# Performance work log

Measured on AMD Instinct MI355X. Metric: run time of the kernel, lower is better.

## Reference

```python
import jax, jax.numpy as jnp
import numpy as np

BATCH, SEQ, IN_DIM, UNITS = 64, 2048, 256, 256


def _glorot(key, shape):
    lim = np.sqrt(6.0 / (shape[0] + shape[1]))
    return jax.random.uniform(key, shape, jnp.float32, -lim, lim)


def setup_inputs() -> dict:
    key = jax.random.key(0)
    ks = jax.random.split(key, 5)
    return {
        "inputs": jax.random.normal(ks[0], (BATCH, SEQ, IN_DIM), jnp.float32),
        "W_f": _glorot(ks[1], (IN_DIM, UNITS)),
        "U_f": _glorot(ks[2], (UNITS, UNITS)),
        "b_f": jnp.zeros((UNITS,), jnp.float32),
        "W_s": _glorot(ks[3], (IN_DIM, UNITS)),
        "U_s": _glorot(ks[4], (UNITS, UNITS)),
        "b_s": jnp.zeros((UNITS,), jnp.float32),
    }


def reference(inputs, W_f, U_f, b_f, W_s, U_s, b_s):
    # Precompute input projections for all timesteps (one big GEMM each).
    xf = jnp.einsum('bti,iu->btu', inputs, W_f) + b_f  # (B, T, U)
    xs = jnp.einsum('bti,iu->btu', inputs, W_s) + b_s  # (B, T, U)

    h0 = jnp.zeros((inputs.shape[0], U_f.shape[0]), inputs.dtype)

    def step(h, xt):
        xf_t, xs_t = xt
        f_t = jax.nn.sigmoid(xf_t + h @ U_f)
        s_tilde = jnp.tanh(xs_t + (f_t * h) @ U_s)
        h_new = (1.0 - f_t) * h + f_t * s_tilde
        return h_new, h_new

    # scan over time: move time axis to front
    _, hs = jax.lax.scan(step, h0, (jnp.swapaxes(xf, 0, 1), jnp.swapaxes(xs, 0, 1)))
    return jnp.swapaxes(hs, 0, 1)  # (B, T, U)
```

## Files before the change

### kernel.cpp

```cpp
#include <hip/hip_runtime.h>
#include <hip/hip_bf16.h>

#define BATCH 64
#define SEQ 2048
#define IN_DIM 256
#define UNITS 256

typedef _Float16 half2_t __attribute__((ext_vector_type(2)));

__device__ __forceinline__ float fdot2(half2_t a, half2_t b, float c) {
#if __has_builtin(__builtin_amdgcn_fdot2)
    return __builtin_amdgcn_fdot2(a, b, c, false);
#else
    return c + (float)a[0] * (float)b[0] + (float)a[1] * (float)b[1];
#endif
}

__device__ __forceinline__ void lds_barrier() {
    asm volatile("s_waitcnt lgkmcnt(0)" ::: "memory");
    __builtin_amdgcn_s_barrier();
    asm volatile("" ::: "memory");
}

__global__ void prep_u(const float* __restrict__ Uf, const float* __restrict__ Us,
                       _Float16* __restrict__ Utf, _Float16* __restrict__ Uts) {
    int idx = blockIdx.x * 256 + threadIdx.x;
    int k = idx >> 8;
    int u = idx & 255;
    Utf[u * 256 + k] = (_Float16)Uf[idx];
    Uts[u * 256 + k] = (_Float16)Us[idx];
}

__global__ __launch_bounds__(256) void proj_kernel(
    const float* __restrict__ X,
    const float* __restrict__ Wf, const float* __restrict__ bf,
    const float* __restrict__ Wsm, const float* __restrict__ bs,
    float* __restrict__ xf_out, _Float16* __restrict__ xs_out)
{
    __shared__ float Xs[64][65];
    __shared__ float Wsh[64][68];

    const int tid = threadIdx.x;
    const int rt = blockIdx.x;
    const int ct = blockIdx.y;
    const int r0 = rt * 64;
    const bool is_f = ct < 4;
    const int c0 = (ct & 3) * 64;
    const float* W = is_f ? Wf : Wsm;
    const float* bias = is_f ? bf : bs;
    const int tx = tid & 15;
    const int ty = tid >> 4;

    float acc[4][4];
#pragma unroll
    for (int i = 0; i < 4; ++i)
#pragma unroll
        for (int j = 0; j < 4; ++j) acc[i][j] = 0.f;

    for (int kc = 0; kc < IN_DIM; kc += 64) {
        __syncthreads();
#pragma unroll
        for (int i = 0; i < 4; ++i) {
            int f = tid + i * 256;
            int row = f >> 4;
            int kq = f & 15;
            float4 v = *(const float4*)(X + (size_t)(r0 + row) * IN_DIM + kc + kq * 4);
            Xs[row][kq * 4 + 0] = v.x;
            Xs[row][kq * 4 + 1] = v.y;
            Xs[row][kq * 4 + 2] = v.z;
            Xs[row][kq * 4 + 3] = v.w;
        }
#pragma unroll
        for (int i = 0; i < 4; ++i) {
            int f = tid + i * 256;
            int kk = f >> 4;
            int n4 = f & 15;
            float4 v = *(const float4*)(W + (size_t)(kc + kk) * UNITS + c0 + n4 * 4);
            *(float4*)&Wsh[kk][n4 * 4] = v;
        }
        __syncthreads();
#pragma unroll 8
        for (int kk = 0; kk < 64; ++kk) {
            float a0 = Xs[tx * 4 + 0][kk];
            float a1 = Xs[tx * 4 + 1][kk];
            float a2 = Xs[tx * 4 + 2][kk];
            float a3 = Xs[tx * 4 + 3][kk];
            float4 bv = *(const float4*)&Wsh[kk][ty * 4];
            acc[0][0] += a0 * bv.x; acc[0][1] += a0 * bv.y; acc[0][2] += a0 * bv.z; acc[0][3] += a0 * bv.w;
            acc[1][0] += a1 * bv.x; acc[1][1] += a1 * bv.y; acc[1][2] += a1 * bv.z; acc[1][3] += a1 * bv.w;
            acc[2][0] += a2 * bv.x; acc[2][1] += a2 * bv.y; acc[2][2] += a2 * bv.z; acc[2][3] += a2 * bv.w;
            acc[3][0] += a3 * bv.x; acc[3][1] += a3 * bv.y; acc[3][2] += a3 * bv.z; acc[3][3] += a3 * bv.w;
        }
    }

#pragma unroll
    for (int i = 0; i < 4; ++i) {
        int r = r0 + tx * 4 + i;
        int n0 = c0 + ty * 4;
        if (is_f) {
            float4 v;
            v.x = acc[i][0] + bias[n0 + 0];
            v.y = acc[i][1] + bias[n0 + 1];
            v.z = acc[i][2] + bias[n0 + 2];
            v.w = acc[i][3] + bias[n0 + 3];
            *(float4*)(xf_out + (size_t)r * UNITS + n0) = v;
        } else {
#pragma unroll
            for (int j = 0; j < 4; ++j)
                xs_out[(size_t)r * UNITS + n0 + j] = (_Float16)(acc[i][j] + bias[n0 + j]);
        }
    }
}

__global__ __launch_bounds__(512, 1) void recur_kernel(
    float* xf_out,
    const _Float16* __restrict__ xs16,
    const _Float16* __restrict__ Utf,
    const _Float16* __restrict__ Uts)
{
    __shared__ __align__(16) _Float16 h2[256];
    __shared__ __align__(16) _Float16 g2[256];

    const int tid = threadIdx.x;
    const int u = tid >> 1;
    const int q = tid & 1;
    const int b = blockIdx.x;

    union F4H { float4 f4; half2_t h[4]; };

    half2_t uf[64], us[64];
    {
        const float4* pf = (const float4*)(Utf + (size_t)u * 256);
        const float4* ps = (const float4*)(Uts + (size_t)u * 256);
#pragma unroll
        for (int j = 0; j < 16; ++j) {
            F4H a; a.f4 = pf[2 * j + q];
            F4H c; c.f4 = ps[2 * j + q];
#pragma unroll
            for (int m = 0; m < 4; ++m) {
                uf[4 * j + m] = a.h[m];
                us[4 * j + m] = c.h[m];
            }
        }
    }

    if (q == 0) h2[u] = (_Float16)0.f;
    float hreg = 0.f;
    __syncthreads();

    const size_t base = (size_t)b * SEQ * UNITS + u;

    float xf0 = xf_out[base];
    float xs0 = (float)xs16[base];
    float xf1 = xf_out[base + UNITS];
    float xs1 = (float)xs16[base + UNITS];

    for (int t = 0; t < SEQ; ++t) {
        float xf2 = 0.f, xs2 = 0.f;
        if (t + 2 < SEQ) {
            xf2 = xf_out[base + (size_t)(t + 2) * UNITS];
            xs2 = (float)xs16[base + (size_t)(t + 2) * UNITS];
        }

        float a0 = 0.f, a1 = 0.f, a2 = 0.f, a3 = 0.f;
        {
            const float4* hv4 = (const float4*)h2;
#pragma unroll
            for (int j = 0; j < 16; ++j) {
                F4H hh; hh.f4 = hv4[2 * j + q];
                a0 = fdot2(uf[4 * j + 0], hh.h[0], a0);
                a1 = fdot2(uf[4 * j + 1], hh.h[1], a1);
                a2 = fdot2(uf[4 * j + 2], hh.h[2], a2);
                a3 = fdot2(uf[4 * j + 3], hh.h[3], a3);
            }
        }
        float af = (a0 + a1) + (a2 + a3);
        af += __shfl_xor(af, 1);
        float f = 1.f / (1.f + __expf(-(xf0 + af)));
        if (q == 0) g2[u] = (_Float16)(f * hreg);
        lds_barrier();

        float c0 = 0.f, c1 = 0.f, c2 = 0.f, c3 = 0.f;
        {
            const float4* gv4 = (const float4*)g2;
#pragma unroll
            for (int j = 0; j < 16; ++j) {
                F4H hh; hh.f4 = gv4[2 * j + q];
                c0 = fdot2(us[4 * j + 0], hh.h[0], c0);
                c1 = fdot2(us[4 * j + 1], hh.h[1], c1);
                c2 = fdot2(us[4 * j + 2], hh.h[2], c2);
                c3 = fdot2(us[4 * j + 3], hh.h[3], c3);
            }
        }
        float as = (c0 + c1) + (c2 + c3);
        as += __shfl_xor(as, 1);
        float z = xs0 + as;
        z = fminf(fmaxf(z, -15.f), 15.f);
        float e = __expf(2.f * z);
        float s = (e - 1.f) / (e + 1.f);
        float hn = (1.f - f) * hreg + f * s;
        hreg = hn;
        if (q == 0) {
            h2[u] = (_Float16)hn;
            xf_out[base + (size_t)t * UNITS] = hn;
        }
        lds_barrier();

        xf0 = xf1; xf1 = xf2;
        xs0 = xs1; xs1 = xs2;
    }
}

extern "C" void kernel_launch(void* const* d_in, const int* in_sizes, int n_in,
                              void* d_out, int out_size, void* d_ws, size_t ws_size,
                              hipStream_t stream) {
    (void)in_sizes; (void)n_in; (void)out_size; (void)ws_size;

    const float* X   = (const float*)d_in[0];
    const float* Wf  = (const float*)d_in[1];
    const float* Uf  = (const float*)d_in[2];
    const float* bf  = (const float*)d_in[3];
    const float* Wsm = (const float*)d_in[4];
    const float* Us  = (const float*)d_in[5];
    const float* bs  = (const float*)d_in[6];
    float* out = (float*)d_out;

    _Float16* xs16 = (_Float16*)d_ws;
    _Float16* Utf  = xs16 + (size_t)BATCH * SEQ * UNITS;
    _Float16* Uts  = Utf + 256 * 256;

    prep_u<<<256, 256, 0, stream>>>(Uf, Us, Utf, Uts);
    proj_kernel<<<dim3(BATCH * SEQ / 64, 8), 256, 0, stream>>>(X, Wf, bf, Wsm, bs, out, xs16);
    recur_kernel<<<BATCH, 512, 0, stream>>>(out, xs16, Utf, Uts);
}
```

Baseline: 3.693 ms.

## Remap recurrence threads to 4 units per 8-lane group for LDS reuse

The recurrent matvec now gives each 8-lane group four output units, with each lane covering a strided eighth of the reduction dimension. Previously each unit used two threads that each read half of h. Each h/g vector loaded from LDS is now reused across four units, which cuts LDS read traffic per step by about four times. The cost is a three-level shuffle reduction instead of one, and only one lane in eight doing the gate math and the vectorized stores, so serial nonlinearity work per thread rises.

```diff
diff --git a/kernel.cpp b/kernel.cpp
--- a/kernel.cpp
+++ b/kernel.cpp
@@ -7,6 +7,7 @@
 #define UNITS 256
 
 typedef _Float16 half2_t __attribute__((ext_vector_type(2)));
+typedef _Float16 half4_t __attribute__((ext_vector_type(4)));
 
 __device__ __forceinline__ float fdot2(half2_t a, half2_t b, float c) {
 #if __has_builtin(__builtin_amdgcn_fdot2)
@@ -122,92 +123,141 @@
     __shared__ __align__(16) _Float16 g2[256];
 
     const int tid = threadIdx.x;
-    const int u = tid >> 1;
-    const int q = tid & 1;
+    const int lane = tid & 63;
+    const int w = tid >> 6;
+    const int q = lane & 7;
+    const int g = lane >> 3;
+    const int U0 = w * 32 + g * 4;
     const int b = blockIdx.x;
 
     union F4H { float4 f4; half2_t h[4]; };
-
-    half2_t uf[64], us[64];
-    {
-        const float4* pf = (const float4*)(Utf + (size_t)u * 256);
-        const float4* ps = (const float4*)(Uts + (size_t)u * 256);
-#pragma unroll
-        for (int j = 0; j < 16; ++j) {
-            F4H a; a.f4 = pf[2 * j + q];
-            F4H c; c.f4 = ps[2 * j + q];
+    union F4A { float4 v; float a[4]; };
+
+    half2_t uf[4][4][4], us[4][4][4];
+#pragma unroll
+    for (int i = 0; i < 4; ++i) {
+        const _Float16* pf = Utf + (size_t)(U0 + i) * 256;
+        const _Float16* ps = Uts + (size_t)(U0 + i) * 256;
+#pragma unroll
+        for (int c = 0; c < 4; ++c) {
+            F4H a; a.f4 = *(const float4*)(pf + c * 64 + q * 8);
+            F4H d; d.f4 = *(const float4*)(ps + c * 64 + q * 8);
 #pragma unroll
             for (int m = 0; m < 4; ++m) {
-                uf[4 * j + m] = a.h[m];
-                us[4 * j + m] = c.h[m];
-            }
-        }
-    }
-
-    if (q == 0) h2[u] = (_Float16)0.f;
-    float hreg = 0.f;
+                uf[i][c][m] = a.h[m];
+                us[i][c][m] = d.h[m];
+            }
+        }
+    }
+
+    float hreg[4] = {0.f, 0.f, 0.f, 0.f};
+    float fg[4]   = {0.f, 0.f, 0.f, 0.f};
+    if (q == 0) {
+        half4_t z;
+        z[0] = (_Float16)0.f; z[1] = (_Float16)0.f;
+        z[2] = (_Float16)0.f; z[3] = (_Float16)0.f;
+        *(half4_t*)(h2 + U0) = z;
+    }
     __syncthreads();
 
-    const size_t base = (size_t)b * SEQ * UNITS + u;
-
-    float xf0 = xf_out[base];
-    float xs0 = (float)xs16[base];
-    float xf1 = xf_out[base + UNITS];
-    float xs1 = (float)xs16[base + UNITS];
+    const size_t base = (size_t)b * SEQ * UNITS + U0;
+
+    F4A xfp0, xfp1;
+    half4_t xsp0, xsp1;
+    xfp0.v = make_float4(0.f, 0.f, 0.f, 0.f);
+    xfp1.v = make_float4(0.f, 0.f, 0.f, 0.f);
+    xsp0 = half4_t{(_Float16)0.f, (_Float16)0.f, (_Float16)0.f, (_Float16)0.f};
+    xsp1 = xsp0;
+    if (q == 0) {
+        xfp0.v = *(const float4*)(xf_out + base);
+        xsp0   = *(const half4_t*)(xs16 + base);
+        xfp1.v = *(const float4*)(xf_out + base + UNITS);
+        xsp1   = *(const half4_t*)(xs16 + base + UNITS);
+    }
 
     for (int t = 0; t < SEQ; ++t) {
-        float xf2 = 0.f, xs2 = 0.f;
-        if (t + 2 < SEQ) {
-            xf2 = xf_out[base + (size_t)(t + 2) * UNITS];
-            xs2 = (float)xs16[base + (size_t)(t + 2) * UNITS];
-        }
-
-        float a0 = 0.f, a1 = 0.f, a2 = 0.f, a3 = 0.f;
+        F4A xfp2; half4_t xsp2;
+        xfp2.v = make_float4(0.f, 0.f, 0.f, 0.f);
+        xsp2 = half4_t{(_Float16)0.f, (_Float16)0.f, (_Float16)0.f, (_Float16)0.f};
+        if (q == 0 && t + 2 < SEQ) {
+            xfp2.v = *(const float4*)(xf_out + base + (size_t)(t + 2) * UNITS);
+            xsp2   = *(const half4_t*)(xs16 + base + (size_t)(t + 2) * UNITS);
+        }
+
+        float acc[4] = {0.f, 0.f, 0.f, 0.f};
         {
             const float4* hv4 = (const float4*)h2;
 #pragma unroll
-            for (int j = 0; j < 16; ++j) {
-                F4H hh; hh.f4 = hv4[2 * j + q];
-                a0 = fdot2(uf[4 * j + 0], hh.h[0], a0);
-                a1 = fdot2(uf[4 * j + 1], hh.h[1], a1);
-                a2 = fdot2(uf[4 * j + 2], hh.h[2], a2);
-                a3 = fdot2(uf[4 * j + 3], hh.h[3], a3);
-            }
-        }
-        float af = (a0 + a1) + (a2 + a3);
-        af += __shfl_xor(af, 1);
-        float f = 1.f / (1.f + __expf(-(xf0 + af)));
-        if (q == 0) g2[u] = (_Float16)(f * hreg);
+            for (int c = 0; c < 4; ++c) {
+                F4H hh; hh.f4 = hv4[c * 8 + q];
+#pragma unroll
+                for (int i = 0; i < 4; ++i) {
+                    acc[i] = fdot2(uf[i][c][0], hh.h[0], acc[i]);
+                    acc[i] = fdot2(uf[i][c][1], hh.h[1], acc[i]);
+                    acc[i] = fdot2(uf[i][c][2], hh.h[2], acc[i]);
+                    acc[i] = fdot2(uf[i][c][3], hh.h[3], acc[i]);
+                }
+            }
+        }
+#pragma unroll
+        for (int i = 0; i < 4; ++i) {
+            acc[i] += __shfl_xor(acc[i], 1);
+            acc[i] += __shfl_xor(acc[i], 2);
+            acc[i] += __shfl_xor(acc[i], 4);
+        }
+        if (q == 0) {
+            half4_t gv;
+#pragma unroll
+            for (int i = 0; i < 4; ++i) {
+                float fv = 1.f / (1.f + __expf(-(xfp0.a[i] + acc[i])));
+                fg[i] = fv;
+                gv[i] = (_Float16)(fv * hreg[i]);
+            }
+            *(half4_t*)(g2 + U0) = gv;
+        }
         lds_barrier();
 
-        float c0 = 0.f, c1 = 0.f, c2 = 0.f, c3 = 0.f;
+        float bcc[4] = {0.f, 0.f, 0.f, 0.f};
         {
             const float4* gv4 = (const float4*)g2;
 #pragma unroll
-            for (int j = 0; j < 16; ++j) {
-                F4H hh; hh.f4 = gv4[2 * j + q];
-                c0 = fdot2(us[4 * j + 0], hh.h[0], c0);
-                c1 = fdot2(us[4 * j + 1], hh.h[1], c1);
-                c2 = fdot2(us[4 * j + 2], hh.h[2], c2);
-                c3 = fdot2(us[4 * j + 3], hh.h[3], c3);
-            }
-        }
-        float as = (c0 + c1) + (c2 + c3);
-        as += __shfl_xor(as, 1);
-        float z = xs0 + as;
-        z = fminf(fmaxf(z, -15.f), 15.f);
-        float e = __expf(2.f * z);
-        float s = (e - 1.f) / (e + 1.f);
-        float hn = (1.f - f) * hreg + f * s;
-        hreg = hn;
+            for (int c = 0; c < 4; ++c) {
+                F4H hh; hh.f4 = gv4[c * 8 + q];
+#pragma unroll
+                for (int i = 0; i < 4; ++i) {
+                    bcc[i] = fdot2(us[i][c][0], hh.h[0], bcc[i]);
+                    bcc[i] = fdot2(us[i][c][1], hh.h[1], bcc[i]);
+                    bcc[i] = fdot2(us[i][c][2], hh.h[2], bcc[i]);
+                    bcc[i] = fdot2(us[i][c][3], hh.h[3], bcc[i]);
+                }
+            }
+        }
+#pragma unroll
+        for (int i = 0; i < 4; ++i) {
+            bcc[i] += __shfl_xor(bcc[i], 1);
+            bcc[i] += __shfl_xor(bcc[i], 2);
+            bcc[i] += __shfl_xor(bcc[i], 4);
+        }
         if (q == 0) {
-            h2[u] = (_Float16)hn;
-            xf_out[base + (size_t)t * UNITS] = hn;
+            half4_t hv; F4A outv;
+#pragma unroll
+            for (int i = 0; i < 4; ++i) {
+                float z = (float)xsp0[i] + bcc[i];
+                z = fminf(fmaxf(z, -15.f), 15.f);
+                float e = __expf(2.f * z);
+                float s = (e - 1.f) / (e + 1.f);
+                float hn = (1.f - fg[i]) * hreg[i] + fg[i] * s;
+                hreg[i] = hn;
+                hv[i] = (_Float16)hn;
+                outv.a[i] = hn;
+            }
+            *(half4_t*)(h2 + U0) = hv;
+            *(float4*)(xf_out + base + (size_t)t * UNITS) = outv.v;
         }
         lds_barrier();
 
-        xf0 = xf1; xf1 = xf2;
-        xs0 = xs1; xs1 = xs2;
+        xfp0 = xfp1; xfp1 = xfp2;
+        xsp0 = xsp1; xsp1 = xsp2;
     }
 }
 
```

After: 4.267 ms. 1.16x slower.
